# Performance work log

Measured on AMD Instinct MI355X. Metric: run time of the kernel, lower is better.

Reference implementation:

```python
import jax, jax.numpy as jnp
import numpy as np

INV_SQRT2 = 0.7071067811865476


def setup_inputs() -> dict:
    key = jax.random.key(0)
    ks = jax.random.split(key, 10)
    B, P, MU = 65536, 2048, 7
    return {
        "dnn_out": jax.random.normal(ks[0], (B, P), jnp.float32),
        "b": jax.random.normal(ks[1], (B,), jnp.float32),
        "h": jax.random.normal(ks[2], (B,), jnp.float32),
        "x_real": jax.random.normal(ks[3], (B, 1), jnp.float32),
        "x_imag": jax.random.normal(ks[4], (B, 1), jnp.float32),
        "ISI_symbols_real": jax.random.normal(ks[5], (B, MU - 1), jnp.float32),
        "ISI_symbols_imag": jax.random.normal(ks[6], (B, MU - 1), jnp.float32),
        "ISI_channels": jax.random.normal(ks[7], (B, MU - 1), jnp.float32),
        "noise": jax.random.normal(ks[8], (B, 1), jnp.float32),
        "prob": jax.random.uniform(ks[9], (1, P), jnp.float32),
        "mu": MU,
        "num_points": P,
        "batch_size": B,
    }


def reference(dnn_out, b, h, x_real, x_imag, ISI_symbols_real, ISI_symbols_imag,
              ISI_channels, noise, prob, mu, num_points, batch_size):
    # Static loop geometry (matches np.floor in the torch code)
    mid = num_points // 2
    T = (num_points // mu) // 2
    num_ISI = mu // 2
    dists = np.arange(-T, T)                                   # [2T] outer dist loop
    w2 = np.array([w for w in range(mu) if w != num_ISI])      # inner mu loop, skip center tap
    offs = (w2 - num_ISI) * 2 * T                              # [mu-1] dnn_out column offsets
    idx = mid + dists[:, None] + offs[None, :]                 # [2T, mu-1]

    # NOTE: in the source, `index` is never incremented, so ALL ISI terms use
    # column 0 of ISI_channels / ISI_symbols. The coefficient is therefore
    # independent of w2 and the w2-sum factors out of the dnn_out gather.
    S = dnn_out[:, idx].sum(-1)                                # [B, 2T] sum over ISI taps

    b1 = b.reshape(-1, 1)                                      # torch reshape (batch,1)
    h1 = h.reshape(-1, 1)
    d0 = dnn_out[:, mid + dists]                               # [B, 2T] center-tap sample

    # A[i,d] = y_rec + noise/sqrt(2) - target  (the j-independent part)
    A_r = b1 * h1 * x_real * d0 + INV_SQRT2 * noise - x_real   # [B, 2T]
    A_i = b1 * h1 * x_imag * d0 + INV_SQRT2 * noise - x_imag

    # torch broadcasting makes y_ISI a [B,B] matrix: entry (i,j) uses
    # b[i]*dnn_out[i,.] and ISI_channels[j,0]*ISI_symbols[j,0]. The mean over
    # the [B,B] matrix of (A_i + b_i*c_j*S_i)^2 is expanded analytically over j
    # to avoid materializing [B,B]: E_j[.] = A^2 + 2*A*bS*E[c] + (bS)^2*E[c^2].
    c_r = ISI_channels[:, 0] * ISI_symbols_real[:, 0]          # [B]
    c_i = ISI_channels[:, 0] * ISI_symbols_imag[:, 0]
    m1r, m2r = jnp.mean(c_r), jnp.mean(c_r ** 2)
    m1i, m2i = jnp.mean(c_i), jnp.mean(c_i ** 2)
    bS = b1 * S                                                # [B, 2T]

    mse_r = jnp.mean(A_r ** 2 + 2.0 * A_r * bS * m1r + bS ** 2 * m2r, axis=0)  # [2T]
    mse_i = jnp.mean(A_i ** 2 + 2.0 * A_i * bS * m1i + bS ** 2 * m2i, axis=0)

    return jnp.sum(prob[0, mid + dists] * (mse_r + mse_i))
```

## Files before the change

### kernel.cpp

```cpp
#include <hip/hip_runtime.h>

#define INV_SQRT2 0.7071067811865476f

__global__ __launch_bounds__(256) void isi_main(
    const float* __restrict__ dnn,
    const float* __restrict__ b,
    const float* __restrict__ h,
    const float* __restrict__ xr,
    const float* __restrict__ xi,
    const float* __restrict__ sym_r,
    const float* __restrict__ sym_i,
    const float* __restrict__ chan,
    const float* __restrict__ noise,
    const float* __restrict__ prob,
    float* __restrict__ ws,
    int B, int P, int D, int MU, int cbase, int midT, int rowsPerBlock)
{
    extern __shared__ float srow[];
    __shared__ float red[8][4];

    const int tid  = threadIdx.x;
    const int wave = tid >> 6;
    const int lane = tid & 63;

    float a0 = 0.f, a1 = 0.f, a2 = 0.f, a3 = 0.f;
    float m0 = 0.f, m1 = 0.f, m2 = 0.f, m3 = 0.f;

    {
        const int gid = blockIdx.x * blockDim.x + tid;
        const int tot = gridDim.x * blockDim.x;
        const int st  = MU - 1;
        for (int i = gid; i < B; i += tot) {
            float ch = chan[(size_t)i * st];
            float cr = ch * sym_r[(size_t)i * st];
            float ci = ch * sym_i[(size_t)i * st];
            m0 += cr; m1 += cr * cr; m2 += ci; m3 += ci * ci;
        }
    }

    const int row0 = blockIdx.x * rowsPerBlock;
    const int row1 = min(B, row0 + rowsPerBlock);
    const int P4   = P >> 2;

    for (int row = row0; row < row1; ++row) {
        const float4* g4 = (const float4*)(dnn + (size_t)row * (size_t)P);
        float4* s4 = (float4*)srow;
        for (int c = tid; c < P4; c += 256) s4[c] = g4[c];
        __syncthreads();

        const float bb   = b[row];
        const float bh   = bb * h[row];
        const float vxr  = xr[row];
        const float vxi  = xi[row];
        const float nz   = INV_SQRT2 * noise[row];
        const float bhxr = bh * vxr;
        const float bhxi = bh * vxi;

        for (int j = tid; j < D; j += 256) {
            float sum7 = 0.f;
            const int c = cbase + j;
            for (int k = 0; k < MU; ++k) sum7 += srow[c + k * D];
            const float d0 = srow[midT + j];
            const float S  = sum7 - d0;
            const float Ar = bhxr * d0 + nz - vxr;
            const float Ai = bhxi * d0 + nz - vxi;
            const float bS = bb * S;
            const float pj = prob[midT + j];
            a0 += pj * (Ar * Ar + Ai * Ai);
            a1 += pj * (Ar * bS);
            a2 += pj * (Ai * bS);
            a3 += pj * (bS * bS);
        }
        __syncthreads();
    }

    float v[8] = {a0, a1, a2, a3, m0, m1, m2, m3};
#pragma unroll
    for (int s = 0; s < 8; ++s) {
        float x = v[s];
#pragma unroll
        for (int off = 32; off > 0; off >>= 1) x += __shfl_down(x, off, 64);
        if (lane == 0) red[s][wave] = x;
    }
    __syncthreads();
    if (tid < 8) {
        float x = red[tid][0] + red[tid][1] + red[tid][2] + red[tid][3];
        atomicAdd(&ws[tid], x);
    }
}

__global__ void isi_final(const float* __restrict__ ws,
                          float* __restrict__ out, int B)
{
    const float invB = 1.0f / (float)B;
    const float P0  = ws[0], P1r = ws[1], P1i = ws[2], P2 = ws[3];
    const float m1r = ws[4] * invB, m2r = ws[5] * invB;
    const float m1i = ws[6] * invB, m2i = ws[7] * invB;
    out[0] = (P0 + 2.0f * (m1r * P1r + m1i * P1i) + (m2r + m2i) * P2) * invB;
}

extern "C" void kernel_launch(void* const* d_in, const int* in_sizes, int n_in,
                              void* d_out, int out_size, void* d_ws, size_t ws_size,
                              hipStream_t stream)
{
    const float* dnn   = (const float*)d_in[0];
    const float* b     = (const float*)d_in[1];
    const float* h     = (const float*)d_in[2];
    const float* xr    = (const float*)d_in[3];
    const float* xi    = (const float*)d_in[4];
    const float* sym_r = (const float*)d_in[5];
    const float* sym_i = (const float*)d_in[6];
    const float* chan  = (const float*)d_in[7];
    const float* noise = (const float*)d_in[8];
    const float* prob  = (const float*)d_in[9];

    const int B  = in_sizes[1];
    const int P  = in_sizes[0] / B;
    const int MU = in_sizes[5] / B + 1;

    const int T      = (P / MU) / 2;
    const int D      = 2 * T;
    const int mid    = P / 2;
    const int midT   = mid - T;
    const int numISI = MU / 2;
    const int cbase  = midT - numISI * D;

    const int rowsPerBlock = 32;
    const int grid = (B + rowsPerBlock - 1) / rowsPerBlock;

    hipMemsetAsync(d_ws, 0, 8 * sizeof(float), stream);

    isi_main<<<grid, 256, P * (int)sizeof(float), stream>>>(
        dnn, b, h, xr, xi, sym_r, sym_i, chan, noise, prob,
        (float*)d_ws, B, P, D, MU, cbase, midT, rowsPerBlock);

    isi_final<<<1, 1, 0, stream>>>((const float*)d_ws, (float*)d_out, B);
}
```

Baseline: 727.4 us.

## Read only needed dnn columns directly, specialize geometry, per-block partials

Drops the shared-memory staging of the full 2048-float row and has each thread read its seven needed columns directly from global memory, so only about 2044 of 2048 columns are touched and the per-row block barriers disappear. A specialized kernel with compile-time geometry uses 320 threads so each output column maps to one thread, and prob is loaded once. Global atomics and the memset are replaced by per-block partials written to the workspace and reduced by a 64-thread final kernel. Rows per block are halved to raise the block count; strided 4-byte loads replace float4 copies, which may reduce load efficiency.

```diff
diff --git a/kernel.cpp b/kernel.cpp
--- a/kernel.cpp
+++ b/kernel.cpp
@@ -2,7 +2,92 @@
 
 #define INV_SQRT2 0.7071067811865476f
 
-__global__ __launch_bounds__(256) void isi_main(
+__global__ __launch_bounds__(320) void isi_main_fast(
+    const float* __restrict__ dnn,
+    const float* __restrict__ b,
+    const float* __restrict__ h,
+    const float* __restrict__ xr,
+    const float* __restrict__ xi,
+    const float* __restrict__ sym_r,
+    const float* __restrict__ sym_i,
+    const float* __restrict__ chan,
+    const float* __restrict__ noise,
+    const float* __restrict__ prob,
+    float* __restrict__ ws,
+    int B, int rowsPerBlock)
+{
+    constexpr int P = 2048, D = 292, cbase = 2, midT = 878;
+
+    const int tid = threadIdx.x;
+    float a0 = 0.f, a1 = 0.f, a2 = 0.f, a3 = 0.f;
+    float m0 = 0.f, m1 = 0.f, m2 = 0.f, m3 = 0.f;
+
+    {
+        const int gid = blockIdx.x * 320 + tid;
+        const int tot = gridDim.x * 320;
+        for (int i = gid; i < B; i += tot) {
+            const float ch = chan[(size_t)i * 6];
+            const float cr = ch * sym_r[(size_t)i * 6];
+            const float ci = ch * sym_i[(size_t)i * 6];
+            m0 += cr; m1 += cr * cr; m2 += ci; m3 += ci * ci;
+        }
+    }
+
+    const int  row0 = blockIdx.x * rowsPerBlock;
+    const int  row1 = min(B, row0 + rowsPerBlock);
+    const bool act  = (tid < D);
+    const float pj  = act ? prob[midT + tid] : 0.f;
+
+#pragma unroll 2
+    for (int row = row0; row < row1; ++row) {
+        const float* __restrict__ rp = dnn + (size_t)row * P;
+        const float bb  = b[row];
+        const float bh  = bb * h[row];
+        const float vxr = xr[row];
+        const float vxi = xi[row];
+        const float nz  = INV_SQRT2 * noise[row];
+        const float cr0 = bh * vxr, ar_c = nz - vxr;
+        const float ci0 = bh * vxi, ai_c = nz - vxi;
+
+        if (act) {
+            const float t0 = rp[cbase + 0 * D + tid];
+            const float t1 = rp[cbase + 1 * D + tid];
+            const float t2 = rp[cbase + 2 * D + tid];
+            const float d0 = rp[cbase + 3 * D + tid];
+            const float t4 = rp[cbase + 4 * D + tid];
+            const float t5 = rp[cbase + 5 * D + tid];
+            const float t6 = rp[cbase + 6 * D + tid];
+
+            const float S  = t0 + t1 + t2 + t4 + t5 + t6;
+            const float Ar = cr0 * d0 + ar_c;
+            const float Ai = ci0 * d0 + ai_c;
+            const float bS = bb * S;
+            a0 += pj * (Ar * Ar + Ai * Ai);
+            a1 += pj * (Ar * bS);
+            a2 += pj * (Ai * bS);
+            a3 += pj * (bS * bS);
+        }
+    }
+
+    __shared__ float red[8][5];
+    float v[8] = {a0, a1, a2, a3, m0, m1, m2, m3};
+    const int wave = tid >> 6, lane = tid & 63;
+#pragma unroll
+    for (int s = 0; s < 8; ++s) {
+        float x = v[s];
+#pragma unroll
+        for (int off = 32; off > 0; off >>= 1) x += __shfl_down(x, off, 64);
+        if (lane == 0) red[s][wave] = x;
+    }
+    __syncthreads();
+    if (tid < 8) {
+        float x = red[tid][0] + red[tid][1] + red[tid][2]
+                + red[tid][3] + red[tid][4];
+        ws[(size_t)blockIdx.x * 8 + tid] = x;
+    }
+}
+
+__global__ __launch_bounds__(256) void isi_main_generic(
     const float* __restrict__ dnn,
     const float* __restrict__ b,
     const float* __restrict__ h,
@@ -16,54 +101,43 @@
     float* __restrict__ ws,
     int B, int P, int D, int MU, int cbase, int midT, int rowsPerBlock)
 {
-    extern __shared__ float srow[];
-    __shared__ float red[8][4];
-
-    const int tid  = threadIdx.x;
-    const int wave = tid >> 6;
-    const int lane = tid & 63;
-
+    const int tid = threadIdx.x;
     float a0 = 0.f, a1 = 0.f, a2 = 0.f, a3 = 0.f;
     float m0 = 0.f, m1 = 0.f, m2 = 0.f, m3 = 0.f;
-
+    const int st = MU - 1;
     {
-        const int gid = blockIdx.x * blockDim.x + tid;
-        const int tot = gridDim.x * blockDim.x;
-        const int st  = MU - 1;
+        const int gid = blockIdx.x * 256 + tid;
+        const int tot = gridDim.x * 256;
         for (int i = gid; i < B; i += tot) {
-            float ch = chan[(size_t)i * st];
-            float cr = ch * sym_r[(size_t)i * st];
-            float ci = ch * sym_i[(size_t)i * st];
+            const float ch = chan[(size_t)i * st];
+            const float cr = ch * sym_r[(size_t)i * st];
+            const float ci = ch * sym_i[(size_t)i * st];
             m0 += cr; m1 += cr * cr; m2 += ci; m3 += ci * ci;
         }
     }
-
     const int row0 = blockIdx.x * rowsPerBlock;
     const int row1 = min(B, row0 + rowsPerBlock);
-    const int P4   = P >> 2;
+    const int nISI = MU / 2;
 
     for (int row = row0; row < row1; ++row) {
-        const float4* g4 = (const float4*)(dnn + (size_t)row * (size_t)P);
-        float4* s4 = (float4*)srow;
-        for (int c = tid; c < P4; c += 256) s4[c] = g4[c];
-        __syncthreads();
-
-        const float bb   = b[row];
-        const float bh   = bb * h[row];
-        const float vxr  = xr[row];
-        const float vxi  = xi[row];
-        const float nz   = INV_SQRT2 * noise[row];
-        const float bhxr = bh * vxr;
-        const float bhxi = bh * vxi;
-
+        const float* __restrict__ rp = dnn + (size_t)row * P;
+        const float bb  = b[row];
+        const float bh  = bb * h[row];
+        const float vxr = xr[row];
+        const float vxi = xi[row];
+        const float nz  = INV_SQRT2 * noise[row];
+        const float cr0 = bh * vxr, ar_c = nz - vxr;
+        const float ci0 = bh * vxi, ai_c = nz - vxi;
         for (int j = tid; j < D; j += 256) {
-            float sum7 = 0.f;
-            const int c = cbase + j;
-            for (int k = 0; k < MU; ++k) sum7 += srow[c + k * D];
-            const float d0 = srow[midT + j];
+            float sum7 = 0.f, d0 = 0.f;
+            for (int k = 0; k < MU; ++k) {
+                const float t = rp[cbase + k * D + j];
+                sum7 += t;
+                if (k == nISI) d0 = t;
+            }
             const float S  = sum7 - d0;
-            const float Ar = bhxr * d0 + nz - vxr;
-            const float Ai = bhxi * d0 + nz - vxi;
+            const float Ar = cr0 * d0 + ar_c;
+            const float Ai = ci0 * d0 + ai_c;
             const float bS = bb * S;
             const float pj = prob[midT + j];
             a0 += pj * (Ar * Ar + Ai * Ai);
@@ -71,10 +145,11 @@
             a2 += pj * (Ai * bS);
             a3 += pj * (bS * bS);
         }
-        __syncthreads();
-    }
-
+    }
+
+    __shared__ float red[8][4];
     float v[8] = {a0, a1, a2, a3, m0, m1, m2, m3};
+    const int wave = tid >> 6, lane = tid & 63;
 #pragma unroll
     for (int s = 0; s < 8; ++s) {
         float x = v[s];
@@ -85,18 +160,35 @@
     __syncthreads();
     if (tid < 8) {
         float x = red[tid][0] + red[tid][1] + red[tid][2] + red[tid][3];
-        atomicAdd(&ws[tid], x);
+        ws[(size_t)blockIdx.x * 8 + tid] = x;
     }
 }
 
 __global__ void isi_final(const float* __restrict__ ws,
-                          float* __restrict__ out, int B)
-{
-    const float invB = 1.0f / (float)B;
-    const float P0  = ws[0], P1r = ws[1], P1i = ws[2], P2 = ws[3];
-    const float m1r = ws[4] * invB, m2r = ws[5] * invB;
-    const float m1i = ws[6] * invB, m2i = ws[7] * invB;
-    out[0] = (P0 + 2.0f * (m1r * P1r + m1i * P1i) + (m2r + m2i) * P2) * invB;
+                          float* __restrict__ out, int nblk, int B)
+{
+    const int lane = threadIdx.x;
+    float v[8] = {0.f, 0.f, 0.f, 0.f, 0.f, 0.f, 0.f, 0.f};
+    for (int i = lane; i < nblk; i += 64) {
+        const float* p = ws + (size_t)i * 8;
+#pragma unroll
+        for (int s = 0; s < 8; ++s) v[s] += p[s];
+    }
+#pragma unroll
+    for (int s = 0; s < 8; ++s) {
+        float x = v[s];
+#pragma unroll
+        for (int off = 32; off > 0; off >>= 1) x += __shfl_down(x, off, 64);
+        v[s] = x;
+    }
+    if (lane == 0) {
+        const float invB = 1.0f / (float)B;
+        const float P0 = v[0], P1r = v[1], P1i = v[2], P2 = v[3];
+        const float m1r = v[4] * invB, m2r = v[5] * invB;
+        const float m1i = v[6] * invB, m2i = v[7] * invB;
+        out[0] = (P0 + 2.0f * (m1r * P1r + m1i * P1i)
+                  + (m2r + m2i) * P2) * invB;
+    }
 }
 
 extern "C" void kernel_launch(void* const* d_in, const int* in_sizes, int n_in,
@@ -118,21 +210,23 @@
     const int P  = in_sizes[0] / B;
     const int MU = in_sizes[5] / B + 1;
 
-    const int T      = (P / MU) / 2;
-    const int D      = 2 * T;
-    const int mid    = P / 2;
-    const int midT   = mid - T;
-    const int numISI = MU / 2;
-    const int cbase  = midT - numISI * D;
-
-    const int rowsPerBlock = 32;
+    const int T     = (P / MU) / 2;
+    const int D     = 2 * T;
+    const int mid   = P / 2;
+    const int midT  = mid - T;
+    const int cbase = midT - (MU / 2) * D;
+
+    const int rowsPerBlock = 16;
     const int grid = (B + rowsPerBlock - 1) / rowsPerBlock;
 
-    hipMemsetAsync(d_ws, 0, 8 * sizeof(float), stream);
-
-    isi_main<<<grid, 256, P * (int)sizeof(float), stream>>>(
-        dnn, b, h, xr, xi, sym_r, sym_i, chan, noise, prob,
-        (float*)d_ws, B, P, D, MU, cbase, midT, rowsPerBlock);
-
-    isi_final<<<1, 1, 0, stream>>>((const float*)d_ws, (float*)d_out, B);
-}
+    if (P == 2048 && MU == 7 && D == 292 && cbase == 2 && midT == 878) {
+        isi_main_fast<<<grid, 320, 0, stream>>>(
+            dnn, b, h, xr, xi, sym_r, sym_i, chan, noise, prob,
+            (float*)d_ws, B, rowsPerBlock);
+    } else {
+        isi_main_generic<<<grid, 256, 0, stream>>>(
+            dnn, b, h, xr, xi, sym_r, sym_i, chan, noise, prob,
+            (float*)d_ws, B, P, D, MU, cbase, midT, rowsPerBlock);
+    }
+    isi_final<<<1, 64, 0, stream>>>((const float*)d_ws, (float*)d_out, grid, B);
+}
```

Measured after the change: 725.8 us. No clear change (-0.2%).
